# Performance work log

Measured on AMD Instinct MI355X. Metric: run time of the kernel, lower is better.

## Reference

```python
import jax, jax.numpy as jnp
import numpy as np

DIM = 2048
BATCH = 64


def setup_inputs() -> dict:
    key = jax.random.key(0)
    kx, kq, kk, kv = jax.random.split(key, 4)
    s = 1.0 / np.sqrt(DIM).astype(np.float32)  # keep q*k logits O(1)
    x = jax.random.normal(kx, (BATCH, DIM), dtype=jnp.float32)
    Wq = jax.random.normal(kq, (DIM, DIM), dtype=jnp.float32) * s
    Wk = jax.random.normal(kk, (DIM, DIM), dtype=jnp.float32) * s
    Wv = jax.random.normal(kv, (DIM, DIM), dtype=jnp.float32) * s
    return {"x": x, "Wq": Wq, "Wk": Wk, "Wv": Wv}


def reference(x, Wq, Wk, Wv):
    # nn.Linear(dim, inner_dim, bias=False): y = x @ W.T, W: [inner_dim, dim]
    q = x @ Wq.T  # [b, N]  (head_dim = 1, so each token's q is a scalar)
    k = x @ Wk.T  # [b, N]
    v = x @ Wv.T  # [b, N]
    # dot[b,i,j] = q[b,i] * k[b,j]  (rank-1 outer product per batch)
    logits = q[:, :, None] * k[:, None, :]  # [b, N, N]
    attn = jax.nn.softmax(logits, axis=-1)
    out = jnp.einsum("bij,bj->bi", attn, v)  # [b, N]
    # dim == inner_dim -> scale is Identity
    return out
```

## Files before the change

### kernel.cpp

```cpp
#include <hip/hip_runtime.h>
#include <hip/hip_bf16.h>

#define DIM 2048
#define NB  64
#define KSL 8
#define JSL 4

typedef __attribute__((ext_vector_type(8))) short bf16x8;
typedef __attribute__((ext_vector_type(4))) float f32x4;
typedef __attribute__((ext_vector_type(2))) float f32x2;

__device__ __forceinline__ unsigned short f32_to_bf16_rne(float f) {
  unsigned u = __builtin_bit_cast(unsigned, f);
  unsigned r = u + 0x7FFF + ((u >> 16) & 1);
  return (unsigned short)(r >> 16);
}

__global__ __launch_bounds__(256)
void prep(const float* __restrict__ x, unsigned short* __restrict__ xhi,
          unsigned short* __restrict__ xlo) {
  const int idx = (blockIdx.x * 256 + threadIdx.x) * 4;
  float4 f = *(const float4*)(x + idx);
  float vf[4] = {f.x, f.y, f.z, f.w};
  ushort4 h4, l4;
  unsigned short* hp = &h4.x;
  unsigned short* lp = &l4.x;
#pragma unroll
  for (int u = 0; u < 4; ++u) {
    unsigned short h = f32_to_bf16_rne(vf[u]);
    float hf = __builtin_bit_cast(float, ((unsigned)h) << 16);
    hp[u] = h;
    lp[u] = f32_to_bf16_rne(vf[u] - hf);
  }
  *(ushort4*)(xhi + idx) = h4;
  *(ushort4*)(xlo + idx) = l4;
}

__global__ __launch_bounds__(256)
void qkv_mfma(const unsigned short* __restrict__ xhi,
              const unsigned short* __restrict__ xlo,
              const float* __restrict__ Wq, const float* __restrict__ Wk,
              const float* __restrict__ Wv, float* __restrict__ part) {
  const int mat = blockIdx.z;
  const float* __restrict__ W = (mat == 0) ? Wq : ((mat == 1) ? Wk : Wv);
  const int t = threadIdx.x;
  const int wave = t >> 6, lane = t & 63;
  const int l15 = lane & 15, quad = lane >> 4;
  const int jt = blockIdx.x * 2 + (wave & 1);
  const int mhalf = wave >> 1;
  const int kb0 = blockIdx.y * (DIM / KSL);

  const float* __restrict__ wrow = W + (size_t)(jt * 16 + l15) * DIM + quad * 8;

  f32x4 acc[2] = {{0.f,0.f,0.f,0.f},{0.f,0.f,0.f,0.f}};

#pragma unroll 2
  for (int kk = 0; kk < DIM / KSL; kk += 32) {
    const int kb = kb0 + kk;
    float4 w0 = *(const float4*)(wrow + kb);
    float4 w1 = *(const float4*)(wrow + kb + 4);
    float wf[8] = {w0.x, w0.y, w0.z, w0.w, w1.x, w1.y, w1.z, w1.w};
    bf16x8 wh, wl;
#pragma unroll
    for (int u = 0; u < 8; ++u) {
      unsigned short h = f32_to_bf16_rne(wf[u]);
      float hf = __builtin_bit_cast(float, ((unsigned)h) << 16);
      wh[u] = (short)h;
      wl[u] = (short)f32_to_bf16_rne(wf[u] - hf);
    }
#pragma unroll
    for (int u = 0; u < 2; ++u) {
      const int mt = mhalf * 2 + u;
      const size_t xoff = (size_t)(mt * 16 + l15) * DIM + kb + quad * 8;
      bf16x8 ah = *(const bf16x8*)(xhi + xoff);
      bf16x8 al = *(const bf16x8*)(xlo + xoff);
      acc[u] = __builtin_amdgcn_mfma_f32_16x16x32_bf16(ah, wh, acc[u], 0, 0, 0);
      acc[u] = __builtin_amdgcn_mfma_f32_16x16x32_bf16(al, wh, acc[u], 0, 0, 0);
      acc[u] = __builtin_amdgcn_mfma_f32_16x16x32_bf16(ah, wl, acc[u], 0, 0, 0);
    }
  }

  float* __restrict__ pbase =
      part + ((size_t)(blockIdx.y * 3 + mat) * NB) * DIM + jt * 16 + l15;
#pragma unroll
  for (int u = 0; u < 2; ++u)
#pragma unroll
    for (int r = 0; r < 4; ++r) {
      const int b = (mhalf * 2 + u) * 16 + quad * 4 + r;
      pbase[(size_t)b * DIM] = acc[u][r];
    }
}

__global__ __launch_bounds__(256)
void attn(const float* __restrict__ part, f32x2* __restrict__ pnd) {
  const int b = blockIdx.z;
  const int js = blockIdx.y;
  const int t = threadIdx.x;
  const int i = blockIdx.x * 256 + t;
  const int jb = js * (DIM / JSL);

  __shared__ __align__(16) float ks[DIM / JSL];
  __shared__ __align__(16) float vs[DIM / JSL];

  const int j2 = t * 2;
  float kx = 0.f, ky = 0.f, vx = 0.f, vy = 0.f;
#pragma unroll
  for (int sl = 0; sl < KSL; ++sl) {
    const float* __restrict__ pk = part + ((size_t)(sl * 3 + 1) * NB + b) * DIM + jb;
    const float* __restrict__ pv = part + ((size_t)(sl * 3 + 2) * NB + b) * DIM + jb;
    float2 a = *(const float2*)(pk + j2);
    float2 c2 = *(const float2*)(pv + j2);
    kx += a.x; ky += a.y; vx += c2.x; vy += c2.y;
  }
  *(float2*)(ks + j2) = make_float2(kx, ky);
  *(float2*)(vs + j2) = make_float2(vx, vy);

  float qi = 0.f;
#pragma unroll
  for (int sl = 0; sl < KSL; ++sl)
    qi += part[((size_t)(sl * 3 + 0) * NB + b) * DIM + i];

  __syncthreads();
  const float c = qi * 1.4426950408889634f;
  const f32x2 cc = {c, c};

  f32x2 num0 = {0.f, 0.f}, num1 = {0.f, 0.f};
  f32x2 den0 = {0.f, 0.f}, den1 = {0.f, 0.f};
#pragma unroll 2
  for (int j = 0; j < DIM / JSL; j += 8) {
    float4 k0 = *(const float4*)(ks + j);
    float4 k1 = *(const float4*)(ks + j + 4);
    float4 v0 = *(const float4*)(vs + j);
    float4 v1 = *(const float4*)(vs + j + 4);
    f32x2 e0, e1, e2, e3;
    e0.x = __builtin_amdgcn_exp2f(c * k0.x);
    e0.y = __builtin_amdgcn_exp2f(c * k0.y);
    e1.x = __builtin_amdgcn_exp2f(c * k0.z);
    e1.y = __builtin_amdgcn_exp2f(c * k0.w);
    e2.x = __builtin_amdgcn_exp2f(c * k1.x);
    e2.y = __builtin_amdgcn_exp2f(c * k1.y);
    e3.x = __builtin_amdgcn_exp2f(c * k1.z);
    e3.y = __builtin_amdgcn_exp2f(c * k1.w);
    den0 += e0; den1 += e1; den0 += e2; den1 += e3;
    f32x2 va = {v0.x, v0.y}, vb = {v0.z, v0.w};
    f32x2 vc = {v1.x, v1.y}, vd = {v1.z, v1.w};
    num0 = __builtin_elementwise_fma(e0, va, num0);
    num1 = __builtin_elementwise_fma(e1, vb, num1);
    num0 = __builtin_elementwise_fma(e2, vc, num0);
    num1 = __builtin_elementwise_fma(e3, vd, num1);
  }
  f32x2 nd;
  nd.x = (num0.x + num0.y) + (num1.x + num1.y);
  nd.y = (den0.x + den0.y) + (den1.x + den1.y);
  pnd[((size_t)b * JSL + js) * DIM + i] = nd;
}

__global__ __launch_bounds__(256)
void attn_fin(const f32x2* __restrict__ pnd, float* __restrict__ out) {
  const int b = blockIdx.y;
  const int i = blockIdx.x * 256 + threadIdx.x;
  float n = 0.f, d = 0.f;
#pragma unroll
  for (int s = 0; s < JSL; ++s) {
    f32x2 p = pnd[((size_t)b * JSL + s) * DIM + i];
    n += p.x; d += p.y;
  }
  out[(size_t)b * DIM + i] = n / d;
}

extern "C" void kernel_launch(void* const* d_in, const int* in_sizes, int n_in,
                              void* d_out, int out_size, void* d_ws, size_t ws_size,
                              hipStream_t stream) {
  const float* x  = (const float*)d_in[0];
  const float* Wq = (const float*)d_in[1];
  const float* Wk = (const float*)d_in[2];
  const float* Wv = (const float*)d_in[3];
  float* out = (float*)d_out;

  char* w = (char*)d_ws;
  unsigned short* xhi = (unsigned short*)w;
  unsigned short* xlo = (unsigned short*)(w + (512 << 10));
  float* part = (float*)(w + (1 << 20));
  f32x2* pnd  = (f32x2*)(w + (16 << 20));

  hipLaunchKernelGGL(prep, dim3(128), dim3(256), 0, stream, x, xhi, xlo);
  hipLaunchKernelGGL(qkv_mfma, dim3(64, KSL, 3), dim3(256), 0, stream,
                     xhi, xlo, Wq, Wk, Wv, part);
  hipLaunchKernelGGL(attn, dim3(8, JSL, NB), dim3(256), 0, stream, part, pnd);
  hipLaunchKernelGGL(attn_fin, dim3(8, NB), dim3(256), 0, stream, pnd, out);
}
```

Baseline: 153.7 us.

## Fuse attention split-j reduction into single kernel and truncate weight hi-part

The attention kernel now handles the full key range per block, which removes the JSL split, the partial num/den buffer and the separate finalize launch. Each block sums the K/V slices for all 2048 keys into shared memory and writes out = num/den directly. The weight hi-part split now truncates instead of rounding, and the lo term still captures the residual. The GEMM and exp loops get larger unroll factors. The trade-off is fewer attention blocks (512 instead of 2048) and 4x redundant K/V slice reduction per batch across the 8 i-blocks.

```diff
diff --git a/kernel.cpp b/kernel.cpp
--- a/kernel.cpp
+++ b/kernel.cpp
@@ -4,7 +4,6 @@
 #define DIM 2048
 #define NB  64
 #define KSL 8
-#define JSL 4
 
 typedef __attribute__((ext_vector_type(8))) short bf16x8;
 typedef __attribute__((ext_vector_type(4))) float f32x4;
@@ -54,7 +53,7 @@
 
   f32x4 acc[2] = {{0.f,0.f,0.f,0.f},{0.f,0.f,0.f,0.f}};
 
-#pragma unroll 2
+#pragma unroll 4
   for (int kk = 0; kk < DIM / KSL; kk += 32) {
     const int kb = kb0 + kk;
     float4 w0 = *(const float4*)(wrow + kb);
@@ -63,9 +62,9 @@
     bf16x8 wh, wl;
 #pragma unroll
     for (int u = 0; u < 8; ++u) {
-      unsigned short h = f32_to_bf16_rne(wf[u]);
-      float hf = __builtin_bit_cast(float, ((unsigned)h) << 16);
-      wh[u] = (short)h;
+      unsigned uu = __builtin_bit_cast(unsigned, wf[u]);
+      wh[u] = (short)(uu >> 16);
+      float hf = __builtin_bit_cast(float, uu & 0xFFFF0000u);
       wl[u] = (short)f32_to_bf16_rne(wf[u] - hf);
     }
 #pragma unroll
@@ -92,28 +91,31 @@
 }
 
 __global__ __launch_bounds__(256)
-void attn(const float* __restrict__ part, f32x2* __restrict__ pnd) {
-  const int b = blockIdx.z;
-  const int js = blockIdx.y;
+void attn(const float* __restrict__ part, float* __restrict__ out) {
+  const int b = blockIdx.y;
   const int t = threadIdx.x;
   const int i = blockIdx.x * 256 + t;
-  const int jb = js * (DIM / JSL);
 
-  __shared__ __align__(16) float ks[DIM / JSL];
-  __shared__ __align__(16) float vs[DIM / JSL];
+  __shared__ __align__(16) float ks[DIM];
+  __shared__ __align__(16) float vs[DIM];
 
-  const int j2 = t * 2;
-  float kx = 0.f, ky = 0.f, vx = 0.f, vy = 0.f;
 #pragma unroll
-  for (int sl = 0; sl < KSL; ++sl) {
-    const float* __restrict__ pk = part + ((size_t)(sl * 3 + 1) * NB + b) * DIM + jb;
-    const float* __restrict__ pv = part + ((size_t)(sl * 3 + 2) * NB + b) * DIM + jb;
-    float2 a = *(const float2*)(pk + j2);
-    float2 c2 = *(const float2*)(pv + j2);
-    kx += a.x; ky += a.y; vx += c2.x; vy += c2.y;
+  for (int j0 = 0; j0 < DIM; j0 += 512) {
+    const int j2 = j0 + t * 2;
+    float kx = 0.f, ky = 0.f, vx = 0.f, vy = 0.f;
+#pragma unroll
+    for (int sl = 0; sl < KSL; ++sl) {
+      const float* __restrict__ pk =
+          part + ((size_t)(sl * 3 + 1) * NB + b) * DIM;
+      const float* __restrict__ pv =
+          part + ((size_t)(sl * 3 + 2) * NB + b) * DIM;
+      float2 a = *(const float2*)(pk + j2);
+      float2 c2 = *(const float2*)(pv + j2);
+      kx += a.x; ky += a.y; vx += c2.x; vy += c2.y;
+    }
+    *(float2*)(ks + j2) = make_float2(kx, ky);
+    *(float2*)(vs + j2) = make_float2(vx, vy);
   }
-  *(float2*)(ks + j2) = make_float2(kx, ky);
-  *(float2*)(vs + j2) = make_float2(vx, vy);
 
   float qi = 0.f;
 #pragma unroll
@@ -122,12 +124,11 @@
 
   __syncthreads();
   const float c = qi * 1.4426950408889634f;
-  const f32x2 cc = {c, c};
 
   f32x2 num0 = {0.f, 0.f}, num1 = {0.f, 0.f};
   f32x2 den0 = {0.f, 0.f}, den1 = {0.f, 0.f};
-#pragma unroll 2
-  for (int j = 0; j < DIM / JSL; j += 8) {
+#pragma unroll 4
+  for (int j = 0; j < DIM; j += 8) {
     float4 k0 = *(const float4*)(ks + j);
     float4 k1 = *(const float4*)(ks + j + 4);
     float4 v0 = *(const float4*)(vs + j);
@@ -149,23 +150,9 @@
     num0 = __builtin_elementwise_fma(e2, vc, num0);
     num1 = __builtin_elementwise_fma(e3, vd, num1);
   }
-  f32x2 nd;
-  nd.x = (num0.x + num0.y) + (num1.x + num1.y);
-  nd.y = (den0.x + den0.y) + (den1.x + den1.y);
-  pnd[((size_t)b * JSL + js) * DIM + i] = nd;
-}
-
-__global__ __launch_bounds__(256)
-void attn_fin(const f32x2* __restrict__ pnd, float* __restrict__ out) {
-  const int b = blockIdx.y;
-  const int i = blockIdx.x * 256 + threadIdx.x;
-  float n = 0.f, d = 0.f;
-#pragma unroll
-  for (int s = 0; s < JSL; ++s) {
-    f32x2 p = pnd[((size_t)b * JSL + s) * DIM + i];
-    n += p.x; d += p.y;
-  }
-  out[(size_t)b * DIM + i] = n / d;
+  const float num = (num0.x + num0.y) + (num1.x + num1.y);
+  const float den = (den0.x + den0.y) + (den1.x + den1.y);
+  out[(size_t)b * DIM + i] = num / den;
 }
 
 extern "C" void kernel_launch(void* const* d_in, const int* in_sizes, int n_in,
@@ -181,11 +168,9 @@
   unsigned short* xhi = (unsigned short*)w;
   unsigned short* xlo = (unsigned short*)(w + (512 << 10));
   float* part = (float*)(w + (1 << 20));
-  f32x2* pnd  = (f32x2*)(w + (16 << 20));
 
   hipLaunchKernelGGL(prep, dim3(128), dim3(256), 0, stream, x, xhi, xlo);
   hipLaunchKernelGGL(qkv_mfma, dim3(64, KSL, 3), dim3(256), 0, stream,
                      xhi, xlo, Wq, Wk, Wv, part);
-  hipLaunchKernelGGL(attn, dim3(8, JSL, NB), dim3(256), 0, stream, part, pnd);
-  hipLaunchKernelGGL(attn_fin, dim3(8, NB), dim3(256), 0, stream, pnd, out);
+  hipLaunchKernelGGL(attn, dim3(8, NB), dim3(256), 0, stream, part, out);
 }
```

Result: slower. 163.5 us (+6.4%).

## Pre-swizzle x into MFMA fragment layout, stage W in LDS, add QKV reduce kernel

Applied to the files above, without the earlier changes.

The prep kernel now writes the bf16 hi/lo split of x directly in the per-lane MFMA fragment order, so each lane's A-operand load becomes one contiguous 16-byte access. The QKV GEMM loads a 32x256 W tile with coalesced row reads, splits it into hi/lo by truncation instead of round-to-nearest, and stores it in LDS for fragment reads. A separate kernel sums the K-split partials once, so attn no longer re-reduces 8 partials for every block, and the attn inner loop's unroll factor goes from 2 to 4. The costs are an extra launch, an LDS sync, and a small change in how the low-order bits of W are split.

```diff
diff --git a/kernel.cpp b/kernel.cpp
--- a/kernel.cpp
+++ b/kernel.cpp
@@ -4,11 +4,13 @@
 #define DIM 2048
 #define NB  64
 #define KSL 8
+#define KT  256
 #define JSL 4
 
-typedef __attribute__((ext_vector_type(8))) short bf16x8;
-typedef __attribute__((ext_vector_type(4))) float f32x4;
-typedef __attribute__((ext_vector_type(2))) float f32x2;
+typedef short bf16x8 __attribute__((ext_vector_type(8)));
+typedef short s16x4  __attribute__((ext_vector_type(4)));
+typedef float f32x4  __attribute__((ext_vector_type(4)));
+typedef float f32x2  __attribute__((ext_vector_type(2)));
 
 __device__ __forceinline__ unsigned short f32_to_bf16_rne(float f) {
   unsigned u = __builtin_bit_cast(unsigned, f);
@@ -17,28 +19,33 @@
 }
 
 __global__ __launch_bounds__(256)
-void prep(const float* __restrict__ x, unsigned short* __restrict__ xhi,
-          unsigned short* __restrict__ xlo) {
-  const int idx = (blockIdx.x * 256 + threadIdx.x) * 4;
-  float4 f = *(const float4*)(x + idx);
+void prep(const float* __restrict__ x, unsigned short* __restrict__ xrh,
+          unsigned short* __restrict__ xrl) {
+  const int tg = blockIdx.x * 256 + threadIdx.x;
+  const int b = tg >> 9;
+  const int k = (tg & 511) * 4;
+  float4 f = *(const float4*)(x + (size_t)b * DIM + k);
+  const int mt = b >> 4, l15 = b & 15;
+  const int ck = k >> 5, quad = (k >> 3) & 3, u = k & 7;
+  const size_t off = (((size_t)(mt * 64 + ck) * 64) + quad * 16 + l15) * 8 + u;
   float vf[4] = {f.x, f.y, f.z, f.w};
   ushort4 h4, l4;
   unsigned short* hp = &h4.x;
   unsigned short* lp = &l4.x;
 #pragma unroll
-  for (int u = 0; u < 4; ++u) {
-    unsigned short h = f32_to_bf16_rne(vf[u]);
+  for (int e = 0; e < 4; ++e) {
+    unsigned short h = f32_to_bf16_rne(vf[e]);
     float hf = __builtin_bit_cast(float, ((unsigned)h) << 16);
-    hp[u] = h;
-    lp[u] = f32_to_bf16_rne(vf[u] - hf);
-  }
-  *(ushort4*)(xhi + idx) = h4;
-  *(ushort4*)(xlo + idx) = l4;
-}
-
-__global__ __launch_bounds__(256)
-void qkv_mfma(const unsigned short* __restrict__ xhi,
-              const unsigned short* __restrict__ xlo,
+    hp[e] = h;
+    lp[e] = f32_to_bf16_rne(vf[e] - hf);
+  }
+  *(ushort4*)(xrh + off) = h4;
+  *(ushort4*)(xrl + off) = l4;
+}
+
+__global__ __launch_bounds__(256)
+void qkv_mfma(const unsigned short* __restrict__ xrh,
+              const unsigned short* __restrict__ xrl,
               const float* __restrict__ Wq, const float* __restrict__ Wk,
               const float* __restrict__ Wv, float* __restrict__ part) {
   const int mat = blockIdx.z;
@@ -46,87 +53,93 @@
   const int t = threadIdx.x;
   const int wave = t >> 6, lane = t & 63;
   const int l15 = lane & 15, quad = lane >> 4;
-  const int jt = blockIdx.x * 2 + (wave & 1);
-  const int mhalf = wave >> 1;
-  const int kb0 = blockIdx.y * (DIM / KSL);
-
-  const float* __restrict__ wrow = W + (size_t)(jt * 16 + l15) * DIM + quad * 8;
-
+  const int j0 = blockIdx.x * 32;
+  const int kb0 = blockIdx.y * KT;
+
+  __shared__ short wh[32][264];
+  __shared__ short wl[32][264];
+
+#pragma unroll
+  for (int p = 0; p < 8; ++p) {
+    const int r = p * 4 + wave;
+    float4 w4 = *(const float4*)(W + (size_t)(j0 + r) * DIM + kb0 + lane * 4);
+    float wf[4] = {w4.x, w4.y, w4.z, w4.w};
+    s16x4 h4, l4;
+#pragma unroll
+    for (int e = 0; e < 4; ++e) {
+      unsigned uu = __builtin_bit_cast(unsigned, wf[e]);
+      h4[e] = (short)(uu >> 16);
+      float hf = __builtin_bit_cast(float, uu & 0xFFFF0000u);
+      float res = wf[e] - hf;
+      l4[e] = (short)(__builtin_bit_cast(unsigned, res) >> 16);
+    }
+    *(s16x4*)&wh[r][lane * 4] = h4;
+    *(s16x4*)&wl[r][lane * 4] = l4;
+  }
+  __syncthreads();
+
+  const int jh = wave & 1;
+  const int mh = wave >> 1;
   f32x4 acc[2] = {{0.f,0.f,0.f,0.f},{0.f,0.f,0.f,0.f}};
 
-#pragma unroll 2
-  for (int kk = 0; kk < DIM / KSL; kk += 32) {
-    const int kb = kb0 + kk;
-    float4 w0 = *(const float4*)(wrow + kb);
-    float4 w1 = *(const float4*)(wrow + kb + 4);
-    float wf[8] = {w0.x, w0.y, w0.z, w0.w, w1.x, w1.y, w1.z, w1.w};
-    bf16x8 wh, wl;
-#pragma unroll
-    for (int u = 0; u < 8; ++u) {
-      unsigned short h = f32_to_bf16_rne(wf[u]);
-      float hf = __builtin_bit_cast(float, ((unsigned)h) << 16);
-      wh[u] = (short)h;
-      wl[u] = (short)f32_to_bf16_rne(wf[u] - hf);
+#pragma unroll
+  for (int kk = 0; kk < 8; ++kk) {
+    bf16x8 whf = *(const bf16x8*)&wh[jh * 16 + l15][kk * 32 + quad * 8];
+    bf16x8 wlf = *(const bf16x8*)&wl[jh * 16 + l15][kk * 32 + quad * 8];
+    const int ck = blockIdx.y * 8 + kk;
+#pragma unroll
+    for (int u = 0; u < 2; ++u) {
+      const int mt = mh * 2 + u;
+      const size_t xo = (((size_t)(mt * 64 + ck)) * 64 + lane) * 8;
+      bf16x8 ah = *(const bf16x8*)(xrh + xo);
+      bf16x8 al = *(const bf16x8*)(xrl + xo);
+      acc[u] = __builtin_amdgcn_mfma_f32_16x16x32_bf16(ah, whf, acc[u], 0, 0, 0);
+      acc[u] = __builtin_amdgcn_mfma_f32_16x16x32_bf16(al, whf, acc[u], 0, 0, 0);
+      acc[u] = __builtin_amdgcn_mfma_f32_16x16x32_bf16(ah, wlf, acc[u], 0, 0, 0);
     }
-#pragma unroll
-    for (int u = 0; u < 2; ++u) {
-      const int mt = mhalf * 2 + u;
-      const size_t xoff = (size_t)(mt * 16 + l15) * DIM + kb + quad * 8;
-      bf16x8 ah = *(const bf16x8*)(xhi + xoff);
-      bf16x8 al = *(const bf16x8*)(xlo + xoff);
-      acc[u] = __builtin_amdgcn_mfma_f32_16x16x32_bf16(ah, wh, acc[u], 0, 0, 0);
-      acc[u] = __builtin_amdgcn_mfma_f32_16x16x32_bf16(al, wh, acc[u], 0, 0, 0);
-      acc[u] = __builtin_amdgcn_mfma_f32_16x16x32_bf16(ah, wl, acc[u], 0, 0, 0);
+  }
+
+  float* __restrict__ pb =
+      part + ((size_t)(blockIdx.y * 3 + mat) * NB) * DIM + j0 + jh * 16 + l15;
+#pragma unroll
+  for (int u = 0; u < 2; ++u)
+#pragma unroll
+    for (int r = 0; r < 4; ++r) {
+      const int b = (mh * 2 + u) * 16 + quad * 4 + r;
+      pb[(size_t)b * DIM] = acc[u][r];
     }
-  }
-
-  float* __restrict__ pbase =
-      part + ((size_t)(blockIdx.y * 3 + mat) * NB) * DIM + jt * 16 + l15;
-#pragma unroll
-  for (int u = 0; u < 2; ++u)
-#pragma unroll
-    for (int r = 0; r < 4; ++r) {
-      const int b = (mhalf * 2 + u) * 16 + quad * 4 + r;
-      pbase[(size_t)b * DIM] = acc[u][r];
-    }
-}
-
-__global__ __launch_bounds__(256)
-void attn(const float* __restrict__ part, f32x2* __restrict__ pnd) {
-  const int b = blockIdx.z;
-  const int js = blockIdx.y;
-  const int t = threadIdx.x;
+}
+
+__global__ __launch_bounds__(256)
+void reduce_qkv(const float* __restrict__ part, float* __restrict__ qkv) {
+  const size_t i2 = ((size_t)blockIdx.x * 256 + threadIdx.x) * 2;
+  float2 s = make_float2(0.f, 0.f);
+#pragma unroll
+  for (int sl = 0; sl < KSL; ++sl) {
+    float2 p = *(const float2*)(part + (size_t)sl * 3 * NB * DIM + i2);
+    s.x += p.x; s.y += p.y;
+  }
+  *(float2*)(qkv + i2) = s;
+}
+
+__global__ __launch_bounds__(256)
+void attn(const float* __restrict__ qkv, f32x2* __restrict__ pnd) {
+  const int b = blockIdx.z, js = blockIdx.y, t = threadIdx.x;
   const int i = blockIdx.x * 256 + t;
-  const int jb = js * (DIM / JSL);
+  const int jb = js * (DIM / JSL), j2 = t * 2;
 
   __shared__ __align__(16) float ks[DIM / JSL];
   __shared__ __align__(16) float vs[DIM / JSL];
 
-  const int j2 = t * 2;
-  float kx = 0.f, ky = 0.f, vx = 0.f, vy = 0.f;
-#pragma unroll
-  for (int sl = 0; sl < KSL; ++sl) {
-    const float* __restrict__ pk = part + ((size_t)(sl * 3 + 1) * NB + b) * DIM + jb;
-    const float* __restrict__ pv = part + ((size_t)(sl * 3 + 2) * NB + b) * DIM + jb;
-    float2 a = *(const float2*)(pk + j2);
-    float2 c2 = *(const float2*)(pv + j2);
-    kx += a.x; ky += a.y; vx += c2.x; vy += c2.y;
-  }
-  *(float2*)(ks + j2) = make_float2(kx, ky);
-  *(float2*)(vs + j2) = make_float2(vx, vy);
-
-  float qi = 0.f;
-#pragma unroll
-  for (int sl = 0; sl < KSL; ++sl)
-    qi += part[((size_t)(sl * 3 + 0) * NB + b) * DIM + i];
-
+  *(float2*)(ks + j2) = *(const float2*)(qkv + ((size_t)(NB + b)) * DIM + jb + j2);
+  *(float2*)(vs + j2) = *(const float2*)(qkv + ((size_t)(2 * NB + b)) * DIM + jb + j2);
+  const float qi = qkv[(size_t)b * DIM + i];
   __syncthreads();
+
   const float c = qi * 1.4426950408889634f;
-  const f32x2 cc = {c, c};
-
   f32x2 num0 = {0.f, 0.f}, num1 = {0.f, 0.f};
   f32x2 den0 = {0.f, 0.f}, den1 = {0.f, 0.f};
-#pragma unroll 2
+#pragma unroll 4
   for (int j = 0; j < DIM / JSL; j += 8) {
     float4 k0 = *(const float4*)(ks + j);
     float4 k1 = *(const float4*)(ks + j + 4);
@@ -178,14 +191,16 @@
   float* out = (float*)d_out;
 
   char* w = (char*)d_ws;
-  unsigned short* xhi = (unsigned short*)w;
-  unsigned short* xlo = (unsigned short*)(w + (512 << 10));
+  unsigned short* xrh = (unsigned short*)w;
+  unsigned short* xrl = (unsigned short*)(w + (512 << 10));
   float* part = (float*)(w + (1 << 20));
-  f32x2* pnd  = (f32x2*)(w + (16 << 20));
-
-  hipLaunchKernelGGL(prep, dim3(128), dim3(256), 0, stream, x, xhi, xlo);
+  float* qkv  = (float*)(w + (16 << 20));
+  f32x2* pnd  = (f32x2*)(w + (20 << 20));
+
+  hipLaunchKernelGGL(prep, dim3(128), dim3(256), 0, stream, x, xrh, xrl);
   hipLaunchKernelGGL(qkv_mfma, dim3(64, KSL, 3), dim3(256), 0, stream,
-                     xhi, xlo, Wq, Wk, Wv, part);
-  hipLaunchKernelGGL(attn, dim3(8, JSL, NB), dim3(256), 0, stream, part, pnd);
+                     xrh, xrl, Wq, Wk, Wv, part);
+  hipLaunchKernelGGL(reduce_qkv, dim3(768), dim3(256), 0, stream, part, qkv);
+  hipLaunchKernelGGL(attn, dim3(8, JSL, NB), dim3(256), 0, stream, qkv, pnd);
   hipLaunchKernelGGL(attn_fin, dim3(8, NB), dim3(256), 0, stream, pnd, out);
 }
```

Result: faster. 140.6 us (-8.5%).
